# Kernel optimization log

Hardware: AMD Instinct MI355X
Metric: run time of the kernel (lower is better)

The kernel has to match this reference:

```python
import jax, jax.numpy as jnp
import numpy as np

NUM_CLASSES = 80
IGNORE_THRESH = 0.7
COORD_SCALE = 1.0
NOOBJ_SCALE = 1.0
OBJ_SCALE = 5.0
CLASS_SCALE = 1.0
NUM_A = 3  # anchors per scale


def iou_cxcywh(a, b):
    """Elementwise/broadcast IoU for boxes in (cx, cy, w, h) format."""
    tl = jnp.maximum(a[..., :2] - a[..., 2:] * 0.5, b[..., :2] - b[..., 2:] * 0.5)
    br = jnp.minimum(a[..., :2] + a[..., 2:] * 0.5, b[..., :2] + b[..., 2:] * 0.5)
    wh = jnp.clip(br - tl, 0.0)
    inter = wh[..., 0] * wh[..., 1]
    union = a[..., 2] * a[..., 3] + b[..., 2] * b[..., 3] - inter
    return inter / union


def yolo_scale_loss(out, targets, anchors):
    B, C, H, W = out.shape
    A, nc = NUM_A, NUM_CLASSES
    HW = H * W
    # ---------------- target building (on detached outputs) ----------------
    od = jax.lax.stop_gradient(out).reshape(B, A, 5 + nc, H, W).transpose(0, 1, 3, 4, 2)  # B,A,H,W,85
    xs = jnp.arange(W, dtype=out.dtype)
    ys = jnp.arange(H, dtype=out.dtype)
    px = jax.nn.sigmoid(od[..., 0]) + xs[None, None, None, :]
    py = jax.nn.sigmoid(od[..., 1]) + ys[None, None, :, None]
    pw = jnp.exp(od[..., 2]) * anchors[:, 0][None, :, None, None]
    ph = jnp.exp(od[..., 3]) * anchors[:, 1][None, :, None, None]
    pred = jnp.stack([px, py, pw, ph], -1).transpose(0, 2, 3, 1, 4)  # B,H,W,A,4
    pred = pred.reshape(B, HW, A, 4)

    Y, X = jnp.meshgrid(jnp.arange(H, dtype=out.dtype), jnp.arange(W, dtype=out.dtype), indexing='ij')
    cell = jnp.stack([X, Y], -1).reshape(HW, 1, 2)  # cell corner (x1y1)
    anc_x1y1 = jnp.concatenate([jnp.broadcast_to(cell, (HW, A, 2)),
                                jnp.broadcast_to(anchors[None], (HW, A, 2))], -1)  # HW,A,4
    anc_xcyc = anc_x1y1.at[..., :2].add(0.5)

    valid = targets.sum(axis=2) > 0  # [B,K] padded-front object mask
    num_obj = valid.sum(axis=1)
    K = targets.shape[1]
    gt = targets[..., :4] * jnp.array([W, H, W, H], dtype=out.dtype)  # grid units
    gt_cls = targets[..., 4].astype(jnp.int32)

    # IoU of every prediction vs every gt: [B, HW*A, K]
    ious = iou_cxcywh(pred.reshape(B, HW * A, 1, 4), gt[:, None, :, :])
    ious = jnp.where(valid[:, None, :], ious, -1.0)
    max_iou = ious.max(-1).reshape(B, HW, A)

    has_pos = (max_iou > IGNORE_THRESH).reshape(B, -1).any(axis=1)
    iou_mask = jnp.full((B, HW, A), NOOBJ_SCALE, dtype=out.dtype)
    iou_mask = jnp.where(has_pos[:, None, None] & (max_iou >= IGNORE_THRESH), 0.0, iou_mask)
    iou_mask = jnp.where((num_obj > 0)[:, None, None], iou_mask, 0.0)

    # per-object responsible cell + anchor
    cx = jnp.clip(jnp.floor(gt[..., 0]), 0, W - 1).astype(jnp.int32)  # [B,K]
    cy = jnp.clip(jnp.floor(gt[..., 1]), 0, H - 1).astype(jnp.int32)
    cell_idx = cy * W + cx
    a_boxes = anc_xcyc[cell_idx]  # [B,K,A,4]
    ov = iou_cxcywh(a_boxes, gt[:, :, None, :])  # [B,K,A]
    a_star = jnp.argmax(ov, -1).astype(jnp.int32)  # [B,K]

    resp = anc_x1y1[cell_idx, a_star]  # [B,K,4] responsible anchor (x1,y1,w,h)
    delta = jnp.stack([gt[..., 0] - resp[..., 0], gt[..., 1] - resp[..., 1],
                       gt[..., 2] / resp[..., 2], gt[..., 3] / resp[..., 3]], -1)  # [B,K,4]
    bidx = jnp.arange(B, dtype=jnp.int32)[:, None]
    obj_iou = max_iou[bidx, cell_idx, a_star]  # [B,K]

    N = B * HW * A
    f = (jnp.arange(B, dtype=jnp.int32)[:, None] * (HW * A) + cell_idx * A + a_star)  # [B,K]
    rank = jnp.arange(B * K, dtype=jnp.int32).reshape(B, K)
    rank_m = jnp.where(valid, rank, -1)
    seg = jax.ops.segment_max(rank_m.ravel(), f.ravel(), num_segments=N)
    winner = valid & (rank == seg[f])
    f_eff = jnp.where(winner, f, N).ravel()  # losers -> dummy slot

    box_target = jnp.zeros((N + 1, 4), out.dtype).at[f_eff].set(delta.reshape(-1, 4))[:-1]
    box_mask = jnp.zeros(N + 1, out.dtype).at[f_eff].set(1.0)[:-1]
    class_target = jnp.zeros(N + 1, jnp.int32).at[f_eff].set(gt_cls.ravel())[:-1]
    class_mask = box_mask
    iou_target = jnp.zeros(N + 1, out.dtype).at[f_eff].set(obj_iou.ravel())[:-1]
    iou_mask = jnp.concatenate([iou_mask.ravel(), jnp.zeros(1, out.dtype)]).at[f_eff].set(OBJ_SCALE)[:-1]

    # ---------------- loss on live outputs ----------------
    o = out.reshape(B, A, 5 + nc, H, W).transpose(0, 3, 4, 1, 2).reshape(N, 5 + nc)
    pred_delta = jnp.concatenate([jax.nn.sigmoid(o[:, :2]), jnp.exp(o[:, 2:4])], axis=1)
    pred_conf = jax.nn.sigmoid(o[:, 4])
    logits = o[:, 5:]

    box_loss = jnp.sum(box_mask[:, None] * (pred_delta - box_target) ** 2)
    iou_loss = jnp.sum((pred_conf * iou_mask - iou_target * iou_mask) ** 2)
    lse = jax.nn.logsumexp(logits, axis=-1)
    tgt_logit = jnp.take_along_axis(logits, class_target[:, None], axis=1)[:, 0]
    class_loss = jnp.sum(class_mask * (lse - tgt_logit))

    return (box_loss * COORD_SCALE / 2.0 + iou_loss / 2.0 + class_loss * CLASS_SCALE) / B


def reference(o1, o2, o3, targets, anchors):
    # anchor_mask = [[6,7,8],[3,4,5],[0,1,2]]
    l1 = yolo_scale_loss(o1, targets, anchors[6:9])
    l2 = yolo_scale_loss(o2, targets, anchors[3:6])
    l3 = yolo_scale_loss(o3, targets, anchors[0:3])
    return (l1 + l2 + l3) / 3.0


def setup_inputs() -> dict:
    key = jax.random.key(0)
    ks = jax.random.split(key, 5)
    B, K, nc = 16, 50, 80
    o1 = jax.random.normal(ks[0], (B, 255, 13, 13), jnp.float32)
    o2 = jax.random.normal(ks[1], (B, 255, 26, 26), jnp.float32)
    o3 = jax.random.normal(ks[2], (B, 255, 52, 52), jnp.float32)
    boxes = jax.random.uniform(ks[3], (B, K, 4), jnp.float32, 0.05, 0.95)
    cls = jax.random.randint(ks[4], (B, K, 1), 0, nc).astype(jnp.float32)
    targets = jnp.concatenate([boxes, cls], axis=-1)
    anchors_px = np.array([[10, 13], [16, 30], [33, 23], [30, 61], [62, 45],
                           [59, 119], [116, 90], [156, 198], [373, 326]], np.float32)
    strides = np.array([8, 8, 8, 16, 16, 16, 32, 32, 32], np.float32)[:, None]
    anchors = jnp.asarray(anchors_px / strides)
    return {"o1": o1, "o2": o2, "o3": o3, "targets": targets, "anchors": anchors}
```

## Files before the change

### kernel.cpp

```cpp
#include <hip/hip_runtime.h>

static constexpr int Bn = 16, Kn = 50, NCn = 80;
static constexpr int NTOT = 16 * 3 * (169 + 676 + 2704);
static constexpr int NBLK_A = (NTOT + 255) / 256;
static constexpr int NBLK_ASSIGN = 12;
static constexpr int NREC = 3 * Bn * Kn;
static constexpr int NBLK_F = NREC / 4;
static constexpr int MIOU_OFF = 0;
static constexpr int HP_OFF   = 170352;
static constexpr int NO_OFF   = 170352 + 48;
static constexpr int S1_OFF   = 170352 + 64;
static constexpr int S2_OFF   = 170352 + 112;
static constexpr int REC_OFF  = 170512;
static constexpr float IGN = 0.7f;
static constexpr float W_BOX = 1.0f / 96.0f;
static constexpr float W_IOU = 1.0f / 96.0f;
static constexpr float W_CLS = 1.0f / 48.0f;

__device__ __forceinline__ float sigf(float x) { return 1.0f / (1.0f + __expf(-x)); }

__device__ __forceinline__ float iou_box(float ax, float ay, float aw, float ah,
                                         float bx, float by, float bw, float bh) {
  float tlx = fmaxf(ax - aw * 0.5f, bx - bw * 0.5f);
  float tly = fmaxf(ay - ah * 0.5f, by - bh * 0.5f);
  float brx = fminf(ax + aw * 0.5f, bx + bw * 0.5f);
  float bry = fminf(ay + ah * 0.5f, by + bh * 0.5f);
  float w = fmaxf(brx - tlx, 0.0f);
  float h = fmaxf(bry - tly, 0.0f);
  float inter = w * h;
  float uni = aw * ah + bw * bh - inter;
  return inter / uni;
}

__device__ __forceinline__ void decode_cell(int g, int& s, int& H, int& HW,
                                            int& base, int& b, int& a, int& hw) {
  if (g < 8112)       { s = 0; H = 13; HW = 169;  base = 0; }
  else if (g < 40560) { s = 1; H = 26; HW = 676;  base = 8112; }
  else                { s = 2; H = 52; HW = 2704; base = 40560; }
  int local = g - base;
  hw = local % HW;
  int t = local / HW;
  a = t % 3;
  b = t / 3;
}

__global__ __launch_bounds__(256) void kMain(const float* __restrict__ o0,
                                             const float* __restrict__ o1,
                                             const float* __restrict__ o2,
                                             const float* __restrict__ tgt,
                                             const float* __restrict__ anc,
                                             float* __restrict__ ws) {
  __shared__ float tg[Bn * Kn * 5];
  __shared__ float ls1[48], ls2[48];
  int tid = threadIdx.x;
  for (int i = tid; i < Bn * Kn * 5; i += 256) tg[i] = tgt[i];
  if (tid < 48) { ls1[tid] = 0.0f; ls2[tid] = 0.0f; }
  __syncthreads();

  if (blockIdx.x >= NBLK_A) {
    int wv = (blockIdx.x - NBLK_A) * 4 + (tid >> 6);
    int lane = tid & 63;
    if (wv >= 48) return;
    int s = wv / 16, b = wv % 16;
    int H, HW, base;
    if (s == 0)      { H = 13; HW = 169;  base = 0; }
    else if (s == 1) { H = 26; HW = 676;  base = 8112; }
    else             { H = 52; HW = 2704; base = 40560; }
    int W = H;
    int aoff = 6 - 3 * s;
    float aw0 = anc[aoff * 2],       ah0 = anc[aoff * 2 + 1];
    float aw1 = anc[(aoff + 1) * 2], ah1 = anc[(aoff + 1) * 2 + 1];
    float aw2 = anc[(aoff + 2) * 2], ah2 = anc[(aoff + 2) * 2 + 1];

    bool valid = false;
    int gslot = -1 - lane;
    float dx = 0, dy = 0, dw = 0, dh = 0, tc = 0;
    if (lane < Kn) {
      const float* tp = &tg[(b * Kn + lane) * 5];
      float tx = tp[0], ty = tp[1], tw = tp[2], th = tp[3];
      tc = tp[4];
      if (tx + ty + tw + th + tc > 0.0f) {
        valid = true;
        float gx = tx * W, gy = ty * H, gw = tw * W, gh = th * H;
        int cx = (int)floorf(gx); cx = min(max(cx, 0), W - 1);
        int cy = (int)floorf(gy); cy = min(max(cy, 0), H - 1);
        float ccx = cx + 0.5f, ccy = cy + 0.5f;
        float i0 = iou_box(ccx, ccy, aw0, ah0, gx, gy, gw, gh);
        float i1 = iou_box(ccx, ccy, aw1, ah1, gx, gy, gw, gh);
        float i2 = iou_box(ccx, ccy, aw2, ah2, gx, gy, gw, gh);
        int astar = 0; float bi = i0;
        if (i1 > bi) { bi = i1; astar = 1; }
        if (i2 > bi) { bi = i2; astar = 2; }
        float raw = (astar == 0) ? aw0 : (astar == 1) ? aw1 : aw2;
        float rah = (astar == 0) ? ah0 : (astar == 1) ? ah1 : ah2;
        gslot = base + (b * 3 + astar) * HW + cy * W + cx;
        dx = gx - (float)cx;
        dy = gy - (float)cy;
        dw = gw / raw;
        dh = gh / rah;
      }
    }
    bool win = valid;
    for (int k2 = 1; k2 < Kn; k2++) {
      int other = __shfl(gslot, k2);
      if (k2 > lane && other == gslot) win = false;
    }
    unsigned long long bal = __ballot(valid);
    if (lane == 0 && s == 0) ((int*)ws)[NO_OFF + b] = (int)__popcll(bal);
    if (lane < Kn) {
      float* r = ws + REC_OFF + (size_t)(wv * Kn + lane) * 8;
      r[0] = win ? 1.0f : 0.0f;
      r[1] = __int_as_float(gslot);
      r[2] = dx; r[3] = dy; r[4] = dw; r[5] = dh;
      r[6] = tc;
      r[7] = 0.0f;
    }
    return;
  }

  int g = blockIdx.x * 256 + tid;
  if (g < NTOT) {
    int s, H, HW, base, b, a, hw;
    decode_cell(g, s, H, HW, base, b, a, hw);
    int W = H;
    const float* o = (s == 0) ? o0 : (s == 1) ? o1 : o2;
    int x = hw % W, y = hw / W;
    int aoff = 6 - 3 * s;
    float aw = anc[(aoff + a) * 2], ah = anc[(aoff + a) * 2 + 1];
    int ob = (b * 255 + a * 85) * HW + hw;
    float px = sigf(o[ob]) + (float)x;
    float py = sigf(o[ob + HW]) + (float)y;
    float pw = __expf(o[ob + 2 * HW]) * aw;
    float ph = __expf(o[ob + 3 * HW]) * ah;
    float conf = sigf(o[ob + 4 * HW]);
    float mi = -1.0f;
    const float* tb = &tg[b * Kn * 5];
    for (int k = 0; k < Kn; k++) {
      float gx = tb[k * 5], gy = tb[k * 5 + 1], gw = tb[k * 5 + 2];
      float gh = tb[k * 5 + 3], gc = tb[k * 5 + 4];
      if (gx + gy + gw + gh + gc > 0.0f) {
        float iou = iou_box(px, py, pw, ph, gx * W, gy * H, gw * W, gh * H);
        mi = fmaxf(mi, iou);
      }
    }
    ws[MIOU_OFF + g] = mi;
    int key = s * 16 + b;
    if (mi > IGN) ((int*)ws)[HP_OFF + key] = 1;
    float c2 = conf * conf;
    atomicAdd(&ls1[key], c2);
    if (mi >= IGN) atomicAdd(&ls2[key], c2);
  }
  __syncthreads();
  if (tid < 48) {
    if (ls1[tid] != 0.0f) atomicAdd(&ws[S1_OFF + tid], ls1[tid]);
    if (ls2[tid] != 0.0f) atomicAdd(&ws[S2_OFF + tid], ls2[tid]);
  }
}

__global__ __launch_bounds__(256) void kFinal(const float* __restrict__ o0,
                                              const float* __restrict__ o1,
                                              const float* __restrict__ o2,
                                              const float* __restrict__ ws,
                                              float* __restrict__ out) {
  __shared__ float wsum[4];
  int tid = threadIdx.x;
  int lane = tid & 63;
  int idx = (blockIdx.x * 256 + tid) >> 6;
  float contrib = 0.0f;

  if (blockIdx.x == 0 && tid < 48) {
    int b = tid % 16;
    int hp = ((const int*)ws)[HP_OFF + tid];
    int nobj = ((const int*)ws)[NO_OFF + b];
    if (nobj > 0) {
      float S1 = ws[S1_OFF + tid], S2 = ws[S2_OFF + tid];
      contrib += (hp ? (S1 - S2) : S1) * W_IOU;
    }
  }

  const float* r = ws + REC_OFF + (size_t)idx * 8;
  float rflag = r[0];
  if (rflag != 0.0f) {
    int g = __float_as_int(r[1]);
    int s, H, HW, base, b, a, hw;
    decode_cell(g, s, H, HW, base, b, a, hw);
    const float* o = (s == 0) ? o0 : (s == 1) ? o1 : o2;
    int ob = (b * 255 + a * 85) * HW + hw;
    float l1 = (lane < NCn) ? o[ob + (5 + lane) * HW] : -1e30f;
    float l2 = (lane + 64 < NCn) ? o[ob + (5 + lane + 64) * HW] : -1e30f;
    float mx = fmaxf(l1, l2);
    for (int off = 32; off > 0; off >>= 1) mx = fmaxf(mx, __shfl_xor(mx, off));
    float sm = __expf(l1 - mx) + __expf(l2 - mx);
    for (int off = 32; off > 0; off >>= 1) sm += __shfl_xor(sm, off);
    if (lane == 0) {
      float lse = mx + __logf(sm);
      int cls = (int)r[6];
      float tgtl = o[ob + (5 + cls) * HW];
      float d0 = sigf(o[ob]) - r[2];
      float d1 = sigf(o[ob + HW]) - r[3];
      float d2 = __expf(o[ob + 2 * HW]) - r[4];
      float d3 = __expf(o[ob + 3 * HW]) - r[5];
      float box = d0 * d0 + d1 * d1 + d2 * d2 + d3 * d3;
      float conf = sigf(o[ob + 4 * HW]);
      float mi = ws[MIOU_OFF + g];
      int hp = ((const int*)ws)[HP_OFF + s * 16 + b];
      float basem = (hp && mi >= IGN) ? 0.0f : 1.0f;
      float vb = conf * basem;
      float dv = 5.0f * (conf - mi);
      float iouc = dv * dv - vb * vb;
      contrib += box * W_BOX + iouc * W_IOU + (lse - tgtl) * W_CLS;
    }
  }

  for (int off = 32; off > 0; off >>= 1) contrib += __shfl_down(contrib, off);
  if (lane == 0) wsum[tid >> 6] = contrib;
  __syncthreads();
  if (tid == 0) {
    float t = wsum[0] + wsum[1] + wsum[2] + wsum[3];
    if (t != 0.0f) atomicAdd(out, t);
  }
}

extern "C" void kernel_launch(void* const* d_in, const int* in_sizes, int n_in,
                              void* d_out, int out_size, void* d_ws, size_t ws_size,
                              hipStream_t stream) {
  const float* o0  = (const float*)d_in[0];
  const float* o1  = (const float*)d_in[1];
  const float* o2  = (const float*)d_in[2];
  const float* tgt = (const float*)d_in[3];
  const float* anc = (const float*)d_in[4];
  float* ws  = (float*)d_ws;
  float* out = (float*)d_out;

  hipMemsetAsync(out, 0, sizeof(float), stream);
  hipMemsetAsync(ws + HP_OFF, 0, 160 * sizeof(float), stream);

  kMain<<<NBLK_A + NBLK_ASSIGN, 256, 0, stream>>>(o0, o1, o2, tgt, anc, ws);
  kFinal<<<NBLK_F, 256, 0, stream>>>(o0, o1, o2, ws, out);
}
```

Before: 122.2 us.

## Replace memsets and global atomics with per-block partials and a final sum kernel

```diff
diff --git a/kernel.cpp b/kernel.cpp
--- a/kernel.cpp
+++ b/kernel.cpp
@@ -7,11 +7,11 @@
 static constexpr int NREC = 3 * Bn * Kn;
 static constexpr int NBLK_F = NREC / 4;
 static constexpr int MIOU_OFF = 0;
-static constexpr int HP_OFF   = 170352;
-static constexpr int NO_OFF   = 170352 + 48;
-static constexpr int S1_OFF   = 170352 + 64;
-static constexpr int S2_OFF   = 170352 + 112;
-static constexpr int REC_OFF  = 170512;
+static constexpr int NO_OFF   = 170352;
+static constexpr int REC_OFF  = 170368;
+static constexpr int EXPC_OFF = 189568;
+static constexpr int EXPD_OFF = 190240;
+static constexpr int PARTF_OFF = 200896;
 static constexpr float IGN = 0.7f;
 static constexpr float W_BOX = 1.0f / 96.0f;
 static constexpr float W_IOU = 1.0f / 96.0f;
@@ -51,16 +51,17 @@
                                              const float* __restrict__ anc,
                                              float* __restrict__ ws) {
   __shared__ float tg[Bn * Kn * 5];
-  __shared__ float ls1[48], ls2[48];
+  __shared__ float ls1[48], ls2[48], lhp[48];
+  __shared__ int lcnt;
   int tid = threadIdx.x;
   for (int i = tid; i < Bn * Kn * 5; i += 256) tg[i] = tgt[i];
-  if (tid < 48) { ls1[tid] = 0.0f; ls2[tid] = 0.0f; }
+  if (tid < 48) { ls1[tid] = 0.0f; ls2[tid] = 0.0f; lhp[tid] = 0.0f; }
+  if (tid == 0) lcnt = 0;
   __syncthreads();
 
   if (blockIdx.x >= NBLK_A) {
     int wv = (blockIdx.x - NBLK_A) * 4 + (tid >> 6);
     int lane = tid & 63;
-    if (wv >= 48) return;
     int s = wv / 16, b = wv % 16;
     int H, HW, base;
     if (s == 0)      { H = 13; HW = 169;  base = 0; }
@@ -133,54 +134,60 @@
     float pw = __expf(o[ob + 2 * HW]) * aw;
     float ph = __expf(o[ob + 3 * HW]) * ah;
     float conf = sigf(o[ob + 4 * HW]);
-    float mi = -1.0f;
+    float pxl = px - pw * 0.5f, pxr = px + pw * 0.5f;
+    float pyl = py - ph * 0.5f, pyr = py + ph * 0.5f;
+    float parea = pw * ph;
+    float bi = -1.0f, bu = 1.0f;
     const float* tb = &tg[b * Kn * 5];
     for (int k = 0; k < Kn; k++) {
       float gx = tb[k * 5], gy = tb[k * 5 + 1], gw = tb[k * 5 + 2];
       float gh = tb[k * 5 + 3], gc = tb[k * 5 + 4];
       if (gx + gy + gw + gh + gc > 0.0f) {
-        float iou = iou_box(px, py, pw, ph, gx * W, gy * H, gw * W, gh * H);
-        mi = fmaxf(mi, iou);
+        float bx = gx * W, by = gy * H, bw = gw * W, bh = gh * H;
+        float tlx = fmaxf(pxl, bx - bw * 0.5f);
+        float tly = fmaxf(pyl, by - bh * 0.5f);
+        float brx = fminf(pxr, bx + bw * 0.5f);
+        float bry = fminf(pyr, by + bh * 0.5f);
+        float w = fmaxf(brx - tlx, 0.0f);
+        float h = fmaxf(bry - tly, 0.0f);
+        float inter = w * h;
+        float uni = parea + bw * bh - inter;
+        if (inter * bu > bi * uni) { bi = inter; bu = uni; }
       }
     }
+    float mi = bi / bu;
     ws[MIOU_OFF + g] = mi;
     int key = s * 16 + b;
-    if (mi > IGN) ((int*)ws)[HP_OFF + key] = 1;
     float c2 = conf * conf;
     atomicAdd(&ls1[key], c2);
     if (mi >= IGN) atomicAdd(&ls2[key], c2);
-  }
-  __syncthreads();
-  if (tid < 48) {
-    if (ls1[tid] != 0.0f) atomicAdd(&ws[S1_OFF + tid], ls1[tid]);
-    if (ls2[tid] != 0.0f) atomicAdd(&ws[S2_OFF + tid], ls2[tid]);
-  }
+    if (mi > IGN) lhp[key] = 1.0f;
+  }
+  __syncthreads();
+  if (tid < 48 && ls1[tid] != 0.0f) {
+    int p = atomicAdd(&lcnt, 1);
+    float* e = ws + EXPD_OFF + (size_t)blockIdx.x * 16 + p * 4;
+    e[0] = __int_as_float(tid);
+    e[1] = ls1[tid];
+    e[2] = ls2[tid];
+    e[3] = lhp[tid];
+  }
+  __syncthreads();
+  if (tid == 0) ((int*)ws)[EXPC_OFF + blockIdx.x] = lcnt;
 }
 
 __global__ __launch_bounds__(256) void kFinal(const float* __restrict__ o0,
                                               const float* __restrict__ o1,
                                               const float* __restrict__ o2,
-                                              const float* __restrict__ ws,
-                                              float* __restrict__ out) {
+                                              float* __restrict__ ws) {
   __shared__ float wsum[4];
   int tid = threadIdx.x;
   int lane = tid & 63;
   int idx = (blockIdx.x * 256 + tid) >> 6;
   float contrib = 0.0f;
 
-  if (blockIdx.x == 0 && tid < 48) {
-    int b = tid % 16;
-    int hp = ((const int*)ws)[HP_OFF + tid];
-    int nobj = ((const int*)ws)[NO_OFF + b];
-    if (nobj > 0) {
-      float S1 = ws[S1_OFF + tid], S2 = ws[S2_OFF + tid];
-      contrib += (hp ? (S1 - S2) : S1) * W_IOU;
-    }
-  }
-
   const float* r = ws + REC_OFF + (size_t)idx * 8;
-  float rflag = r[0];
-  if (rflag != 0.0f) {
+  if (r[0] != 0.0f) {
     int g = __float_as_int(r[1]);
     int s, H, HW, base, b, a, hw;
     decode_cell(g, s, H, HW, base, b, a, hw);
@@ -203,8 +210,7 @@
       float box = d0 * d0 + d1 * d1 + d2 * d2 + d3 * d3;
       float conf = sigf(o[ob + 4 * HW]);
       float mi = ws[MIOU_OFF + g];
-      int hp = ((const int*)ws)[HP_OFF + s * 16 + b];
-      float basem = (hp && mi >= IGN) ? 0.0f : 1.0f;
+      float basem = (mi >= IGN) ? 0.0f : 1.0f;
       float vb = conf * basem;
       float dv = 5.0f * (conf - mi);
       float iouc = dv * dv - vb * vb;
@@ -215,10 +221,40 @@
   for (int off = 32; off > 0; off >>= 1) contrib += __shfl_down(contrib, off);
   if (lane == 0) wsum[tid >> 6] = contrib;
   __syncthreads();
-  if (tid == 0) {
-    float t = wsum[0] + wsum[1] + wsum[2] + wsum[3];
-    if (t != 0.0f) atomicAdd(out, t);
-  }
+  if (tid == 0)
+    ws[PARTF_OFF + blockIdx.x] = wsum[0] + wsum[1] + wsum[2] + wsum[3];
+}
+
+__global__ __launch_bounds__(256) void kSum(const float* __restrict__ ws,
+                                            float* __restrict__ out) {
+  __shared__ float S1L[48], S2L[48], HPL[48];
+  __shared__ float bsum[4];
+  int tid = threadIdx.x;
+  if (tid < 48) { S1L[tid] = 0.0f; S2L[tid] = 0.0f; HPL[tid] = 0.0f; }
+  __syncthreads();
+  for (int bid = tid; bid < NBLK_A; bid += 256) {
+    int cnt = ((const int*)ws)[EXPC_OFF + bid];
+    const float* e = ws + EXPD_OFF + (size_t)bid * 16;
+    for (int j = 0; j < cnt; j++) {
+      int key = __float_as_int(e[j * 4]);
+      atomicAdd(&S1L[key], e[j * 4 + 1]);
+      atomicAdd(&S2L[key], e[j * 4 + 2]);
+      if (e[j * 4 + 3] != 0.0f) HPL[key] = 1.0f;
+    }
+  }
+  __syncthreads();
+  float c = 0.0f;
+  if (tid < 48) {
+    int b = tid & 15;
+    int nobj = ((const int*)ws)[NO_OFF + b];
+    if (nobj > 0)
+      c += ((HPL[tid] > 0.0f) ? (S1L[tid] - S2L[tid]) : S1L[tid]) * W_IOU;
+  }
+  for (int i = tid; i < NBLK_F; i += 256) c += ws[PARTF_OFF + i];
+  for (int off = 32; off > 0; off >>= 1) c += __shfl_down(c, off);
+  if ((tid & 63) == 0) bsum[tid >> 6] = c;
+  __syncthreads();
+  if (tid == 0) out[0] = bsum[0] + bsum[1] + bsum[2] + bsum[3];
 }
 
 extern "C" void kernel_launch(void* const* d_in, const int* in_sizes, int n_in,
@@ -232,9 +268,7 @@
   float* ws  = (float*)d_ws;
   float* out = (float*)d_out;
 
-  hipMemsetAsync(out, 0, sizeof(float), stream);
-  hipMemsetAsync(ws + HP_OFF, 0, 160 * sizeof(float), stream);
-
   kMain<<<NBLK_A + NBLK_ASSIGN, 256, 0, stream>>>(o0, o1, o2, tgt, anc, ws);
-  kFinal<<<NBLK_F, 256, 0, stream>>>(o0, o1, o2, ws, out);
-}
+  kFinal<<<NBLK_F, 256, 0, stream>>>(o0, o1, o2, ws);
+  kSum<<<1, 256, 0, stream>>>(ws, out);
+}
```

After: 116.6 us. 4.5% less time.
